# Kernel optimization log

Measured on AMD Instinct MI355X. Metric: run time of the kernel, lower is better.

## Reference

```python
import jax, jax.numpy as jnp
import numpy as np

C, F, CLS, B, HW = 2048, 512, 200, 128, 14
SCALES = (4, 5, 7, 11)
EPS = 1e-5

def _pool_matrix(n, k):
    # PyTorch AdaptiveAvgPool2d bin edges: [floor(i*n/k), ceil((i+1)*n/k))
    P = np.zeros((k, n), np.float32)
    for i in range(k):
        s = (i * n) // k
        e = -((-(i + 1) * n) // k)
        P[i, s:e] = 1.0 / (e - s)
    return jnp.asarray(P)

_PMATS = [_pool_matrix(HW, k) for k in SCALES]

def _bn(x, g, b):
    # BatchNorm with batch statistics (train-mode), biased variance, eps=1e-5
    m = x.mean(0)
    v = x.var(0)
    return (x - m) * jax.lax.rsqrt(v + EPS) * g + b

def _head(h, g1, b1, w1, bi1, g2, b2, w2, bi2):
    # Sequential(BN, Linear, BN, ELU, Linear)
    h = _bn(h, g1, b1) @ w1.T + bi1
    h = jax.nn.elu(_bn(h, g2, b2))
    return h @ w2.T + bi2

def setup_inputs():
    key = jax.random.key(0)
    ks = iter(jax.random.split(key, 16))
    def rn(shape, scale=0.02):
        return jax.random.normal(next(ks), shape, jnp.float32) * scale
    d = {"x": jax.random.normal(next(ks), (B, C, HW, HW), jnp.float32)}
    d.update(g_bn_g=jnp.ones((C,)), g_bn_b=jnp.zeros((C,)), g_w=rn((4, C)), g_b=jnp.zeros((4,)))
    d.update(e_w=rn((C, C)), e_b=jnp.zeros((C,)), e_g=jnp.ones((C,)), e_bb=jnp.zeros((C,)))
    def head(p, din, dh):
        d[p + "_g1"] = jnp.ones((din,)); d[p + "_b1"] = jnp.zeros((din,))
        d[p + "_w1"] = rn((dh, din));   d[p + "_bi1"] = jnp.zeros((dh,))
        d[p + "_g2"] = jnp.ones((dh,)); d[p + "_b2"] = jnp.zeros((dh,))
        d[p + "_w2"] = rn((CLS, dh));   d[p + "_bi2"] = jnp.zeros((CLS,))
    head("hl", C, F)
    head("hh", C, F)
    head("hf", 2 * C, 2 * F)
    return d

def reference(x, g_bn_g, g_bn_b, g_w, g_b, e_w, e_b, e_g, e_bb,
              hl_g1, hl_b1, hl_w1, hl_bi1, hl_g2, hl_b2, hl_w2, hl_bi2,
              hh_g1, hh_b1, hh_w1, hh_bi1, hh_g2, hh_b2, hh_w2, hh_bi2,
              hf_g1, hf_b1, hf_w1, hf_bi1, hf_g2, hf_b2, hf_w2, hf_bi2):
    # Gate: global max pool -> BN -> ELU -> Linear -> hard gumbel-softmax (temp=1,
    # deterministic/eval: straight-through hard argmax over softmax)
    mp = x.max((2, 3))                                              # [B,C]
    logits = jax.nn.elu(_bn(mp, g_bn_g, g_bn_b)) @ g_w.T + g_b      # [B,4]
    soft = jax.nn.softmax(logits, -1)
    hard = jax.nn.one_hot(jnp.argmax(soft, -1), 4, dtype=soft.dtype)
    gw = jax.lax.stop_gradient(hard - soft) + soft                  # [B,4]
    # multi-scale adaptive avg pool (4,5,7,11) then global max per scale — fully batched
    ms = jnp.stack([jnp.einsum('ki,bcij,lj->bckl', P, x, P).max((2, 3)) for P in _PMATS], -1)  # [B,C,4]
    pool = jnp.einsum('bcs,bs->bc', ms, gw)                         # gated weighted sum
    # expert_low: 1x1 conv on 1x1 spatial == linear, then BN2d(batch stats) + ReLU
    xl = jax.nn.relu(_bn(pool @ e_w.T + e_b, e_g, e_bb))
    # NOTE: source computes expert_high(x) then overwrites with self.max(x) -> x_high = global max pool of x
    xh = mp
    xf = jnp.concatenate([xl, xh], -1)
    out_low = _head(xl, hl_g1, hl_b1, hl_w1, hl_bi1, hl_g2, hl_b2, hl_w2, hl_bi2)
    out_high = _head(xh, hh_g1, hh_b1, hh_w1, hh_bi1, hh_g2, hh_b2, hh_w2, hh_bi2)
    out = _head(xf, hf_g1, hf_b1, hf_w1, hf_bi1, hf_g2, hf_b2, hf_w2, hf_bi2)
    return (out_low, out_high, out)
```

## Files before the change

### kernel.cpp

```cpp
#include <hip/hip_runtime.h>
#include <math.h>

#define B_DIM 128
#define C_DIM 2048
#define HW2   196

__global__ __launch_bounds__(256) void pool_max_kernel(
    const float* __restrict__ x, float* __restrict__ mp, float* __restrict__ ms) {
  __shared__ float lds[4][4][208];
  const int tid  = threadIdx.x;
  const int w    = tid >> 6;
  const int lane = tid & 63;
  const int g    = lane >> 4;
  const int c    = lane & 15;
  const size_t waveBase = (size_t)blockIdx.x * 16 + w * 4;

  const float* src = x + waveBase * HW2;
  #pragma unroll
  for (int j = 0; j < 4; ++j) {
    int f = lane + 64 * j;
    if (f < 196) {
      int t = (f * 669) >> 15;
      float4 v = *(const float4*)(src + f * 4);
      *(float4*)&lds[w][t][(f - 49 * t) * 4] = v;
    }
  }

  float xv[14];
  const float* col = &lds[w][g][c];
  #pragma unroll
  for (int r = 0; r < 14; ++r) xv[r] = col[r * 14];

  float cmax = (c < 14) ? xv[0] : -INFINITY;
  #pragma unroll
  for (int r = 1; r < 14; ++r) if (c < 14) cmax = fmaxf(cmax, xv[r]);
  #pragma unroll
  for (int off = 8; off > 0; off >>= 1) cmax = fmaxf(cmax, __shfl_xor(cmax, off));

  float P[15];
  P[0] = 0.f;
  #pragma unroll
  for (int r = 0; r < 14; ++r) P[r + 1] = P[r] + xv[r];

  float sm0, sm1, sm2, sm3;

  {
    constexpr int rs[4] = {0, 3, 7, 10}, re[4] = {4, 7, 11, 14};
    const bool valid = (0x489u >> c) & 1;
    float vmax = -INFINITY;
    #pragma unroll
    for (int i = 0; i < 4; ++i) {
      float v  = P[re[i]] - P[rs[i]];
      float w2 = v + __shfl_down(v, 1);
      float w4 = w2 + __shfl_down(w2, 2);
      vmax = fmaxf(vmax, valid ? w4 : -INFINITY);
    }
    #pragma unroll
    for (int off = 8; off > 0; off >>= 1) vmax = fmaxf(vmax, __shfl_xor(vmax, off));
    sm0 = vmax * 0.0625f;
  }
  {
    constexpr int rs[5] = {0, 2, 5, 8, 11}, re[5] = {3, 6, 9, 12, 14};
    constexpr float srl[5] = {1.f/3.f, 0.25f, 0.25f, 0.25f, 1.f/3.f};
    const bool valid = (0x925u >> c) & 1;
    const bool is3   = (0x801u >> c) & 1;
    const float invc = is3 ? (1.f/3.f) : 0.25f;
    float vmax = -INFINITY;
    #pragma unroll
    for (int i = 0; i < 5; ++i) {
      float v  = P[re[i]] - P[rs[i]];
      float d1 = __shfl_down(v, 1);
      float d2 = __shfl_down(v, 2);
      float w2 = v + d1;
      float w3 = w2 + d2;
      float w4 = w2 + __shfl_down(w2, 2);
      float wv = (is3 ? w3 : w4) * invc * srl[i];
      vmax = fmaxf(vmax, valid ? wv : -INFINITY);
    }
    #pragma unroll
    for (int off = 8; off > 0; off >>= 1) vmax = fmaxf(vmax, __shfl_xor(vmax, off));
    sm1 = vmax;
  }
  {
    constexpr int rs[7] = {0, 2, 4, 6, 8, 10, 12};
    const bool valid = (0x1555u >> c) & 1;
    float vmax = -INFINITY;
    #pragma unroll
    for (int i = 0; i < 7; ++i) {
      float v  = P[rs[i] + 2] - P[rs[i]];
      float w2 = v + __shfl_down(v, 1);
      vmax = fmaxf(vmax, valid ? w2 : -INFINITY);
    }
    #pragma unroll
    for (int off = 8; off > 0; off >>= 1) vmax = fmaxf(vmax, __shfl_xor(vmax, off));
    sm2 = vmax * 0.25f;
  }
  {
    constexpr int rs[11] = {0, 1, 2, 3, 5, 6, 7, 8, 10, 11, 12};
    constexpr int re[11] = {2, 3, 4, 6, 7, 8, 9, 11, 12, 13, 14};
    constexpr float srl[11] = {0.5f, 0.5f, 0.5f, 1.f/3.f, 0.5f, 0.5f, 0.5f,
                               1.f/3.f, 0.5f, 0.5f, 0.5f};
    const bool valid = (0x1DEFu >> c) & 1;
    const bool is3   = (0x108u >> c) & 1;
    const float invc = is3 ? (1.f/3.f) : 0.5f;
    float vmax = -INFINITY;
    #pragma unroll
    for (int i = 0; i < 11; ++i) {
      float v  = P[re[i]] - P[rs[i]];
      float d1 = __shfl_down(v, 1);
      float d2 = __shfl_down(v, 2);
      float w2 = v + d1;
      float w3 = w2 + d2;
      float wv = (is3 ? w3 : w2) * invc * srl[i];
      vmax = fmaxf(vmax, valid ? wv : -INFINITY);
    }
    #pragma unroll
    for (int off = 8; off > 0; off >>= 1) vmax = fmaxf(vmax, __shfl_xor(vmax, off));
    sm3 = vmax;
  }

  if (c == 0) {
    size_t T = waveBase + g;
    mp[T] = cmax;
    *(float4*)&ms[T * 4] = make_float4(sm0, sm1, sm2, sm3);
  }
}

__global__ __launch_bounds__(256) void statsmp_kernel(
    const float* __restrict__ mp,
    const float* __restrict__ hh_g1, const float* __restrict__ hh_b1,
    const float* __restrict__ hf_g1, const float* __restrict__ hf_b1,
    float* __restrict__ mean_mp, float* __restrict__ rstd_mp,
    float* __restrict__ s_h, float* __restrict__ t_h,
    float* __restrict__ sf2, float* __restrict__ tf2) {
  const int ci = threadIdx.x & 15;
  const int g  = threadIdx.x >> 4;
  const int c  = blockIdx.x * 16 + ci;
  float s = 0.f, q = 0.f;
  #pragma unroll
  for (int r = 0; r < 8; ++r) {
    float v = mp[(size_t)(g * 8 + r) * C_DIM + c];
    s += v; q += v * v;
  }
  __shared__ float ss[16][16], qq[16][16];
  ss[g][ci] = s; qq[g][ci] = q;
  __syncthreads();
  if (g == 0) {
    float S = 0.f, Q = 0.f;
    #pragma unroll
    for (int j = 0; j < 16; ++j) { S += ss[j][ci]; Q += qq[j][ci]; }
    float m = S * (1.f / B_DIM);
    float var = Q * (1.f / B_DIM) - m * m;
    if (var < 0.f) var = 0.f;
    float r = rsqrtf(var + 1e-5f);
    mean_mp[c] = m; rstd_mp[c] = r;
    float a = r * hh_g1[c];        s_h[c] = a; t_h[c] = hh_b1[c] - m * a;
    float b = r * hf_g1[2048 + c]; sf2[c] = b; tf2[c] = hf_b1[2048 + c] - m * b;
  }
}

__global__ void gate_select_kernel(
    const float* __restrict__ mp,
    const float* __restrict__ mean, const float* __restrict__ rstd,
    const float* __restrict__ gg, const float* __restrict__ gb,
    const float* __restrict__ gw, const float* __restrict__ gbias,
    const float* __restrict__ ms, float* __restrict__ pool) {
  const int b = blockIdx.x;
  const int t = threadIdx.x;
  float s0 = 0.f, s1 = 0.f, s2 = 0.f, s3 = 0.f;
  for (int c = t; c < C_DIM; c += 256) {
    float v = mp[(size_t)b * C_DIM + c];
    float xn = (v - mean[c]) * rstd[c] * gg[c] + gb[c];
    float e = xn > 0.f ? xn : expm1f(xn);
    s0 += e * gw[c];
    s1 += e * gw[C_DIM + c];
    s2 += e * gw[2 * C_DIM + c];
    s3 += e * gw[3 * C_DIM + c];
  }
  __shared__ float red[4][256];
  __shared__ int ssel;
  red[0][t] = s0; red[1][t] = s1; red[2][t] = s2; red[3][t] = s3;
  __syncthreads();
  for (int st = 128; st > 0; st >>= 1) {
    if (t < st) {
      red[0][t] += red[0][t + st];
      red[1][t] += red[1][t + st];
      red[2][t] += red[2][t + st];
      red[3][t] += red[3][t + st];
    }
    __syncthreads();
  }
  if (t == 0) {
    float best = red[0][0] + gbias[0];
    int bi = 0;
    for (int j = 1; j < 4; ++j) {
      float l = red[j][0] + gbias[j];
      if (l > best) { best = l; bi = j; }
    }
    ssel = bi;
  }
  __syncthreads();
  const int sel = ssel;
  for (int c = t; c < C_DIM; c += 256)
    pool[(size_t)b * C_DIM + c] = ms[((size_t)b * C_DIM + c) * 4 + sel];
}

__global__ __launch_bounds__(256) void gemm_e_kernel(
    const float* __restrict__ A, const float* __restrict__ W,
    float* __restrict__ P) {
  __shared__ float As[32][68];
  __shared__ float Bs[32][68];
  const int t = threadIdx.x;
  const int m0 = blockIdx.y << 6;
  const int n0 = blockIdx.x << 6;
  const int kbeg = blockIdx.z << 8;
  const int lr = t >> 3;
  const int lk4 = (t & 7) << 2;
  const int tx = t & 15, ty = t >> 4;
  float acc[4][4] = {{0.f}};
  for (int k0 = kbeg; k0 < kbeg + 256; k0 += 32) {
    float4 a0 = *(const float4*)&A[(size_t)(m0 + lr) * 2048 + k0 + lk4];
    float4 a1 = *(const float4*)&A[(size_t)(m0 + lr + 32) * 2048 + k0 + lk4];
    float4 b0 = *(const float4*)&W[(size_t)(n0 + lr) * 2048 + k0 + lk4];
    float4 b1 = *(const float4*)&W[(size_t)(n0 + lr + 32) * 2048 + k0 + lk4];
    __syncthreads();
    As[lk4 + 0][lr] = a0.x; As[lk4 + 1][lr] = a0.y; As[lk4 + 2][lr] = a0.z; As[lk4 + 3][lr] = a0.w;
    As[lk4 + 0][lr + 32] = a1.x; As[lk4 + 1][lr + 32] = a1.y; As[lk4 + 2][lr + 32] = a1.z; As[lk4 + 3][lr + 32] = a1.w;
    Bs[lk4 + 0][lr] = b0.x; Bs[lk4 + 1][lr] = b0.y; Bs[lk4 + 2][lr] = b0.z; Bs[lk4 + 3][lr] = b0.w;
    Bs[lk4 + 0][lr + 32] = b1.x; Bs[lk4 + 1][lr + 32] = b1.y; Bs[lk4 + 2][lr + 32] = b1.z; Bs[lk4 + 3][lr + 32] = b1.w;
    __syncthreads();
    #pragma unroll
    for (int kk = 0; kk < 32; ++kk) {
      float4 av = *(const float4*)&As[kk][ty << 2];
      float4 bv = *(const float4*)&Bs[kk][tx << 2];
      acc[0][0] = fmaf(av.x, bv.x, acc[0][0]); acc[0][1] = fmaf(av.x, bv.y, acc[0][1]);
      acc[0][2] = fmaf(av.x, bv.z, acc[0][2]); acc[0][3] = fmaf(av.x, bv.w, acc[0][3]);
      acc[1][0] = fmaf(av.y, bv.x, acc[1][0]); acc[1][1] = fmaf(av.y, bv.y, acc[1][1]);
      acc[1][2] = fmaf(av.y, bv.z, acc[1][2]); acc[1][3] = fmaf(av.y, bv.w, acc[1][3]);
      acc[2][0] = fmaf(av.z, bv.x, acc[2][0]); acc[2][1] = fmaf(av.z, bv.y, acc[2][1]);
      acc[2][2] = fmaf(av.z, bv.z, acc[2][2]); acc[2][3] = fmaf(av.z, bv.w, acc[2][3]);
      acc[3][0] = fmaf(av.w, bv.x, acc[3][0]); acc[3][1] = fmaf(av.w, bv.y, acc[3][1]);
      acc[3][2] = fmaf(av.w, bv.z, acc[3][2]); acc[3][3] = fmaf(av.w, bv.w, acc[3][3]);
    }
  }
  float* Pz = P + ((size_t)blockIdx.z << 18);
  #pragma unroll
  for (int i = 0; i < 4; ++i) {
    int m = m0 + (ty << 2) + i;
    #pragma unroll
    for (int j = 0; j < 4; ++j)
      Pz[(size_t)m * 2048 + n0 + (tx << 2) + j] = acc[i][j];
  }
}

__global__ __launch_bounds__(256) void expert_fused_kernel(
    const float* __restrict__ Pe, const float* __restrict__ e_b,
    const float* __restrict__ e_g, const float* __restrict__ e_bb,
    const float* __restrict__ hl_g1, const float* __restrict__ hl_b1,
    const float* __restrict__ hf_g1, const float* __restrict__ hf_b1,
    float* __restrict__ xl,
    float* __restrict__ s_l, float* __restrict__ t_l,
    float* __restrict__ sf1, float* __restrict__ tf1) {
  const int ci = threadIdx.x & 15;
  const int g  = threadIdx.x >> 4;
  const int c  = blockIdx.x * 16 + ci;
  float v[8];
  float s = 0.f, q = 0.f;
  const float bias = e_b[c];
  #pragma unroll
  for (int r = 0; r < 8; ++r) {
    const size_t row = g * 8 + r;
    float acc = bias;
    #pragma unroll
    for (int z = 0; z < 8; ++z)
      acc += Pe[((size_t)z << 18) + row * 2048 + c];
    v[r] = acc; s += acc; q += acc * acc;
  }
  __shared__ float ss[16][16], qq[16][16];
  __shared__ float sm[16], sr[16];
  ss[g][ci] = s; qq[g][ci] = q;
  __syncthreads();
  if (g == 0) {
    float S = 0.f, Q = 0.f;
    #pragma unroll
    for (int j = 0; j < 16; ++j) { S += ss[j][ci]; Q += qq[j][ci]; }
    float m = S * (1.f / B_DIM);
    float var = Q * (1.f / B_DIM) - m * m;
    if (var < 0.f) var = 0.f;
    sm[ci] = m; sr[ci] = rsqrtf(var + 1e-5f);
  }
  __syncthreads();
  const float m = sm[ci], rst = sr[ci];
  const float eg = e_g[c], eb2 = e_bb[c];
  float s2 = 0.f, q2 = 0.f;
  #pragma unroll
  for (int r = 0; r < 8; ++r) {
    float xv = fmaxf((v[r] - m) * rst * eg + eb2, 0.f);
    xl[(size_t)(g * 8 + r) * 2048 + c] = xv;
    s2 += xv; q2 += xv * xv;
  }
  __syncthreads();
  ss[g][ci] = s2; qq[g][ci] = q2;
  __syncthreads();
  if (g == 0) {
    float S = 0.f, Q = 0.f;
    #pragma unroll
    for (int j = 0; j < 16; ++j) { S += ss[j][ci]; Q += qq[j][ci]; }
    float mm = S * (1.f / B_DIM);
    float var = Q * (1.f / B_DIM) - mm * mm;
    if (var < 0.f) var = 0.f;
    float rr = rsqrtf(var + 1e-5f);
    float a = rr * hl_g1[c]; s_l[c] = a; t_l[c] = hl_b1[c] - mm * a;
    float b = rr * hf_g1[c]; sf1[c] = b; tf1[c] = hf_b1[c] - mm * b;
  }
}

__global__ __launch_bounds__(256) void gemm_w1_kernel(
    const float* __restrict__ xl, const float* __restrict__ mp,
    const float* __restrict__ s_l, const float* __restrict__ t_l,
    const float* __restrict__ s_h, const float* __restrict__ t_h,
    const float* __restrict__ sf1, const float* __restrict__ tf1,
    const float* __restrict__ sf2, const float* __restrict__ tf2,
    const float* __restrict__ hl_w1, const float* __restrict__ hh_w1,
    const float* __restrict__ hf_w1,
    float* __restrict__ P_l, float* __restrict__ P_h, float* __restrict__ P_f) {
  const int jx = blockIdx.x;
  const int z  = blockIdx.z;
  const float *A, *S, *T, *Wt;
  float* P;
  int N, K, n0, kA, kW, Kc;
  if (jx < 8) {
    N = 512; K = 2048; Kc = 128; Wt = hl_w1; n0 = jx << 6;
    kW = z * 128; kA = kW; A = xl; S = s_l; T = t_l;
    P = P_l + ((size_t)z << 16);
  } else if (jx < 16) {
    N = 512; K = 2048; Kc = 128; Wt = hh_w1; n0 = (jx - 8) << 6;
    kW = z * 128; kA = kW; A = mp; S = s_h; T = t_h;
    P = P_h + ((size_t)z << 16);
  } else {
    N = 1024; K = 4096; Kc = 256; Wt = hf_w1; n0 = (jx - 16) << 6;
    kW = z * 256;
    if (kW >= 2048) { A = mp; S = sf2; T = tf2; kA = kW - 2048; }
    else            { A = xl; S = sf1; T = tf1; kA = kW; }
    P = P_f + ((size_t)z << 17);
  }
  const int m0 = blockIdx.y << 6;
  __shared__ float As[32][68];
  __shared__ float Bs[32][68];
  const int t = threadIdx.x;
  const int lr = t >> 3;
  const int lk4 = (t & 7) << 2;
  const int tx = t & 15, ty = t >> 4;
  float acc[4][4] = {{0.f}};
  for (int k0 = 0; k0 < Kc; k0 += 32) {
    const int ka = kA + k0 + lk4;
    float4 a0 = *(const float4*)&A[(size_t)(m0 + lr) * 2048 + ka];
    float4 a1 = *(const float4*)&A[(size_t)(m0 + lr + 32) * 2048 + ka];
    float4 s4 = *(const float4*)&S[ka];
    float4 t4 = *(const float4*)&T[ka];
    a0.x = fmaf(a0.x, s4.x, t4.x); a0.y = fmaf(a0.y, s4.y, t4.y);
    a0.z = fmaf(a0.z, s4.z, t4.z); a0.w = fmaf(a0.w, s4.w, t4.w);
    a1.x = fmaf(a1.x, s4.x, t4.x); a1.y = fmaf(a1.y, s4.y, t4.y);
    a1.z = fmaf(a1.z, s4.z, t4.z); a1.w = fmaf(a1.w, s4.w, t4.w);
    const int kw = kW + k0 + lk4;
    float4 b0 = *(const float4*)&Wt[(size_t)(n0 + lr) * K + kw];
    float4 b1 = *(const float4*)&Wt[(size_t)(n0 + lr + 32) * K + kw];
    __syncthreads();
    As[lk4 + 0][lr] = a0.x; As[lk4 + 1][lr] = a0.y; As[lk4 + 2][lr] = a0.z; As[lk4 + 3][lr] = a0.w;
    As[lk4 + 0][lr + 32] = a1.x; As[lk4 + 1][lr + 32] = a1.y; As[lk4 + 2][lr + 32] = a1.z; As[lk4 + 3][lr + 32] = a1.w;
    Bs[lk4 + 0][lr] = b0.x; Bs[lk4 + 1][lr] = b0.y; Bs[lk4 + 2][lr] = b0.z; Bs[lk4 + 3][lr] = b0.w;
    Bs[lk4 + 0][lr + 32] = b1.x; Bs[lk4 + 1][lr + 32] = b1.y; Bs[lk4 + 2][lr + 32] = b1.z; Bs[lk4 + 3][lr + 32] = b1.w;
    __syncthreads();
    #pragma unroll
    for (int kk = 0; kk < 32; ++kk) {
      float4 av = *(const float4*)&As[kk][ty << 2];
      float4 bv = *(const float4*)&Bs[kk][tx << 2];
      acc[0][0] = fmaf(av.x, bv.x, acc[0][0]); acc[0][1] = fmaf(av.x, bv.y, acc[0][1]);
      acc[0][2] = fmaf(av.x, bv.z, acc[0][2]); acc[0][3] = fmaf(av.x, bv.w, acc[0][3]);
      acc[1][0] = fmaf(av.y, bv.x, acc[1][0]); acc[1][1] = fmaf(av.y, bv.y, acc[1][1]);
      acc[1][2] = fmaf(av.y, bv.z, acc[1][2]); acc[1][3] = fmaf(av.y, bv.w, acc[1][3]);
      acc[2][0] = fmaf(av.z, bv.x, acc[2][0]); acc[2][1] = fmaf(av.z, bv.y, acc[2][1]);
      acc[2][2] = fmaf(av.z, bv.z, acc[2][2]); acc[2][3] = fmaf(av.z, bv.w, acc[2][3]);
      acc[3][0] = fmaf(av.w, bv.x, acc[3][0]); acc[3][1] = fmaf(av.w, bv.y, acc[3][1]);
      acc[3][2] = fmaf(av.w, bv.z, acc[3][2]); acc[3][3] = fmaf(av.w, bv.w, acc[3][3]);
    }
  }
  #pragma unroll
  for (int i = 0; i < 4; ++i) {
    int m = m0 + (ty << 2) + i;
    #pragma unroll
    for (int j = 0; j < 4; ++j)
      P[(size_t)m * N + n0 + (tx << 2) + j] = acc[i][j];
  }
}

__global__ __launch_bounds__(256) void heads_fused_kernel(
    const float* __restrict__ P_l, const float* __restrict__ P_h,
    const float* __restrict__ P_f,
    const float* __restrict__ bl1, const float* __restrict__ bh1,
    const float* __restrict__ bf1,
    const float* __restrict__ g2l, const float* __restrict__ b2l,
    const float* __restrict__ g2h, const float* __restrict__ b2h,
    const float* __restrict__ g2f, const float* __restrict__ b2f,
    float* __restrict__ a2_l, float* __restrict__ a2_h, float* __restrict__ a2_f) {
  const int ci = threadIdx.x & 15;
  const int g  = threadIdx.x >> 4;
  const int cj = blockIdx.x * 16 + ci;
  const float *P, *bi, *g2, *b2;
  float* out;
  int N, cc;
  if (cj < 512)       { P = P_l; bi = bl1; g2 = g2l; b2 = b2l; out = a2_l; N = 512;  cc = cj; }
  else if (cj < 1024) { P = P_h; bi = bh1; g2 = g2h; b2 = b2h; out = a2_h; N = 512;  cc = cj - 512; }
  else                { P = P_f; bi = bf1; g2 = g2f; b2 = b2f; out = a2_f; N = 1024; cc = cj - 1024; }
  const size_t sstride = (size_t)N * 128;
  float v[8];
  float s = 0.f, q = 0.f;
  const float bias = bi[cc];
  #pragma unroll
  for (int r = 0; r < 8; ++r) {
    const size_t row = g * 8 + r;
    float acc = bias;
    #pragma unroll
    for (int z = 0; z < 16; ++z)
      acc += P[(size_t)z * sstride + row * N + cc];
    v[r] = acc; s += acc; q += acc * acc;
  }
  __shared__ float ss[16][16], qq[16][16];
  __shared__ float sm[16], sr[16];
  ss[g][ci] = s; qq[g][ci] = q;
  __syncthreads();
  if (g == 0) {
    float S = 0.f, Q = 0.f;
    #pragma unroll
    for (int j = 0; j < 16; ++j) { S += ss[j][ci]; Q += qq[j][ci]; }
    float m = S * (1.f / B_DIM);
    float var = Q * (1.f / B_DIM) - m * m;
    if (var < 0.f) var = 0.f;
    sm[ci] = m; sr[ci] = rsqrtf(var + 1e-5f);
  }
  __syncthreads();
  const float m = sm[ci], rr = sr[ci];
  const float gg = g2[cc], bb = b2[cc];
  #pragma unroll
  for (int r = 0; r < 8; ++r) {
    float xn = (v[r] - m) * rr * gg + bb;
    out[(size_t)(g * 8 + r) * N + cc] = xn > 0.f ? xn : expm1f(xn);
  }
}

__global__ __launch_bounds__(256) void gemm_w2_kernel(
    const float* __restrict__ a2_l, const float* __restrict__ a2_h,
    const float* __restrict__ a2_f,
    const float* __restrict__ hl_w2, const float* __restrict__ hh_w2,
    const float* __restrict__ hf_w2,
    float* __restrict__ Pw) {
  const int jx = blockIdx.x;
  const int z  = blockIdx.z;
  const float *A, *Wt;
  int K, Kc, pOff, n0;
  if (jx < 4)      { A = a2_l; Wt = hl_w2; K = 512;  Kc = 64;  pOff = 0;     n0 = jx << 6; }
  else if (jx < 8) { A = a2_h; Wt = hh_w2; K = 512;  Kc = 64;  pOff = 25600; n0 = (jx - 4) << 6; }
  else             { A = a2_f; Wt = hf_w2; K = 1024; Kc = 128; pOff = 51200; n0 = (jx - 8) << 6; }
  const int kbeg = z * Kc;
  const int m0 = blockIdx.y << 6;
  __shared__ float As[32][68];
  __shared__ float Bs[32][68];
  const int t = threadIdx.x;
  const int lr = t >> 3;
  const int lk4 = (t & 7) << 2;
  const int tx = t & 15, ty = t >> 4;
  float acc[4][4] = {{0.f}};
  const float4 z4 = make_float4(0.f, 0.f, 0.f, 0.f);
  for (int k0 = kbeg; k0 < kbeg + Kc; k0 += 32) {
    float4 a0 = *(const float4*)&A[(size_t)(m0 + lr) * K + k0 + lk4];
    float4 a1 = *(const float4*)&A[(size_t)(m0 + lr + 32) * K + k0 + lk4];
    int n1 = n0 + lr, n2 = n0 + lr + 32;
    float4 b0 = (n1 < 200) ? *(const float4*)&Wt[(size_t)n1 * K + k0 + lk4] : z4;
    float4 b1 = (n2 < 200) ? *(const float4*)&Wt[(size_t)n2 * K + k0 + lk4] : z4;
    __syncthreads();
    As[lk4 + 0][lr] = a0.x; As[lk4 + 1][lr] = a0.y; As[lk4 + 2][lr] = a0.z; As[lk4 + 3][lr] = a0.w;
    As[lk4 + 0][lr + 32] = a1.x; As[lk4 + 1][lr + 32] = a1.y; As[lk4 + 2][lr + 32] = a1.z; As[lk4 + 3][lr + 32] = a1.w;
    Bs[lk4 + 0][lr] = b0.x; Bs[lk4 + 1][lr] = b0.y; Bs[lk4 + 2][lr] = b0.z; Bs[lk4 + 3][lr] = b0.w;
    Bs[lk4 + 0][lr + 32] = b1.x; Bs[lk4 + 1][lr + 32] = b1.y; Bs[lk4 + 2][lr + 32] = b1.z; Bs[lk4 + 3][lr + 32] = b1.w;
    __syncthreads();
    #pragma unroll
    for (int kk = 0; kk < 32; ++kk) {
      float4 av = *(const float4*)&As[kk][ty << 2];
      float4 bv = *(const float4*)&Bs[kk][tx << 2];
      acc[0][0] = fmaf(av.x, bv.x, acc[0][0]); acc[0][1] = fmaf(av.x, bv.y, acc[0][1]);
      acc[0][2] = fmaf(av.x, bv.z, acc[0][2]); acc[0][3] = fmaf(av.x, bv.w, acc[0][3]);
      acc[1][0] = fmaf(av.y, bv.x, acc[1][0]); acc[1][1] = fmaf(av.y, bv.y, acc[1][1]);
      acc[1][2] = fmaf(av.y, bv.z, acc[1][2]); acc[1][3] = fmaf(av.y, bv.w, acc[1][3]);
      acc[2][0] = fmaf(av.z, bv.x, acc[2][0]); acc[2][1] = fmaf(av.z, bv.y, acc[2][1]);
      acc[2][2] = fmaf(av.z, bv.z, acc[2][2]); acc[2][3] = fmaf(av.z, bv.w, acc[2][3]);
      acc[3][0] = fmaf(av.w, bv.x, acc[3][0]); acc[3][1] = fmaf(av.w, bv.y, acc[3][1]);
      acc[3][2] = fmaf(av.w, bv.z, acc[3][2]); acc[3][3] = fmaf(av.w, bv.w, acc[3][3]);
    }
  }
  float* Pz = Pw + (size_t)z * 76800 + pOff;
  #pragma unroll
  for (int i = 0; i < 4; ++i) {
    int m = m0 + (ty << 2) + i;
    #pragma unroll
    for (int j = 0; j < 4; ++j) {
      int n = n0 + (tx << 2) + j;
      if (n < 200) Pz[(size_t)m * 200 + n] = acc[i][j];
    }
  }
}

__global__ void reduce_out_kernel(const float* __restrict__ P,
                                  const float* __restrict__ bl,
                                  const float* __restrict__ bh,
                                  const float* __restrict__ bf,
                                  float* __restrict__ out) {
  int i = blockIdx.x * 256 + threadIdx.x;
  if (i >= 76800) return;
  int job = i / 25600;
  int n = (i - job * 25600) % 200;
  float s = (job == 0) ? bl[n] : (job == 1) ? bh[n] : bf[n];
  for (int z = 0; z < 8; ++z) s += P[(size_t)z * 76800 + i];
  out[i] = s;
}

extern "C" void kernel_launch(void* const* d_in, const int* in_sizes, int n_in,
                              void* d_out, int out_size, void* d_ws, size_t ws_size,
                              hipStream_t stream) {
  const float* x      = (const float*)d_in[0];
  const float* g_bn_g = (const float*)d_in[1];
  const float* g_bn_b = (const float*)d_in[2];
  const float* g_w    = (const float*)d_in[3];
  const float* g_b    = (const float*)d_in[4];
  const float* e_w    = (const float*)d_in[5];
  const float* e_b    = (const float*)d_in[6];
  const float* e_g    = (const float*)d_in[7];
  const float* e_bb   = (const float*)d_in[8];
  const float* hl_g1  = (const float*)d_in[9];
  const float* hl_b1  = (const float*)d_in[10];
  const float* hl_w1  = (const float*)d_in[11];
  const float* hl_bi1 = (const float*)d_in[12];
  const float* hl_g2  = (const float*)d_in[13];
  const float* hl_b2  = (const float*)d_in[14];
  const float* hl_w2  = (const float*)d_in[15];
  const float* hl_bi2 = (const float*)d_in[16];
  const float* hh_g1  = (const float*)d_in[17];
  const float* hh_b1  = (const float*)d_in[18];
  const float* hh_w1  = (const float*)d_in[19];
  const float* hh_bi1 = (const float*)d_in[20];
  const float* hh_g2  = (const float*)d_in[21];
  const float* hh_b2  = (const float*)d_in[22];
  const float* hh_w2  = (const float*)d_in[23];
  const float* hh_bi2 = (const float*)d_in[24];
  const float* hf_g1  = (const float*)d_in[25];
  const float* hf_b1  = (const float*)d_in[26];
  const float* hf_w1  = (const float*)d_in[27];
  const float* hf_bi1 = (const float*)d_in[28];
  const float* hf_g2  = (const float*)d_in[29];
  const float* hf_b2  = (const float*)d_in[30];
  const float* hf_w2  = (const float*)d_in[31];
  const float* hf_bi2 = (const float*)d_in[32];
  float* out = (float*)d_out;

  float* W = (float*)d_ws;
  const size_t BC = (size_t)B_DIM * C_DIM;
  float* mp   = W;
  float* ms   = mp + BC;
  float* pool = ms + BC * 4;
  float* xl   = pool + BC;
  float* a2_l = xl + BC;
  float* a2_h = a2_l + 128 * 512;
  float* a2_f = a2_h + 128 * 512;
  float* st   = a2_f + 128 * 1024;
  float* mean_mp = st;           float* rstd_mp = st + 2048;
  float* s_h  = st + 2 * 2048;   float* t_h  = st + 3 * 2048;
  float* sf2  = st + 4 * 2048;   float* tf2  = st + 5 * 2048;
  float* s_l  = st + 6 * 2048;   float* t_l  = st + 7 * 2048;
  float* sf1  = st + 8 * 2048;   float* tf1  = st + 9 * 2048;
  float* P_e  = st + 10 * 2048;
  float* P_l2 = P_e + 8 * BC;
  float* P_hh = P_l2 + (size_t)16 * 65536;
  float* P_f  = P_hh + (size_t)16 * 65536;
  float* P_w2 = P_e;

  pool_max_kernel<<<16384, 256, 0, stream>>>(x, mp, ms);

  statsmp_kernel<<<128, 256, 0, stream>>>(mp, hh_g1, hh_b1, hf_g1, hf_b1,
                                          mean_mp, rstd_mp, s_h, t_h, sf2, tf2);

  gate_select_kernel<<<128, 256, 0, stream>>>(mp, mean_mp, rstd_mp, g_bn_g, g_bn_b,
                                              g_w, g_b, ms, pool);

  gemm_e_kernel<<<dim3(32, 2, 8), 256, 0, stream>>>(pool, e_w, P_e);

  expert_fused_kernel<<<128, 256, 0, stream>>>(P_e, e_b, e_g, e_bb,
                                               hl_g1, hl_b1, hf_g1, hf_b1,
                                               xl, s_l, t_l, sf1, tf1);

  gemm_w1_kernel<<<dim3(32, 2, 16), 256, 0, stream>>>(
      xl, mp, s_l, t_l, s_h, t_h, sf1, tf1, sf2, tf2,
      hl_w1, hh_w1, hf_w1, P_l2, P_hh, P_f);

  heads_fused_kernel<<<128, 256, 0, stream>>>(
      P_l2, P_hh, P_f, hl_bi1, hh_bi1, hf_bi1,
      hl_g2, hl_b2, hh_g2, hh_b2, hf_g2, hf_b2,
      a2_l, a2_h, a2_f);

  gemm_w2_kernel<<<dim3(12, 2, 8), 256, 0, stream>>>(
      a2_l, a2_h, a2_f, hl_w2, hh_w2, hf_w2, P_w2);

  reduce_out_kernel<<<300, 256, 0, stream>>>(P_w2, hl_bi2, hh_bi2, hf_bi2, out);
}
```

Baseline: 158.6 us.

## Port expert and head-W1 GEMMs to bf16 MFMA with swizzled LDS tiles

Replaces the fp32 FMA tiled GEMMs for the expert linear and the three head first-layer linears with bf16 MFMA 16x16x32 kernels. Each block now covers all 128 batch rows with XOR-swizzled LDS tiles, converting fp32 inputs to bf16 on load. The grid drops the M dimension but keeps split-K. This aims to cut the ALU cost of the small GEMMs, at the price of bf16 rounding of activations and weights, which risks accuracy against the fp32 reference.

```diff
diff --git a/kernel.cpp b/kernel.cpp
--- a/kernel.cpp
+++ b/kernel.cpp
@@ -4,6 +4,15 @@
 #define B_DIM 128
 #define C_DIM 2048
 #define HW2   196
+
+typedef __attribute__((ext_vector_type(8))) short bf16x8;
+typedef __attribute__((ext_vector_type(4))) float f32x4;
+
+__device__ __forceinline__ unsigned short f2bf(float f) {
+  unsigned u = __float_as_uint(f);
+  u += 0x7FFFu + ((u >> 16) & 1u);
+  return (unsigned short)(u >> 16);
+}
 
 __global__ __launch_bounds__(256) void pool_max_kernel(
     const float* __restrict__ x, float* __restrict__ mp, float* __restrict__ ms) {
@@ -205,51 +214,103 @@
     pool[(size_t)b * C_DIM + c] = ms[((size_t)b * C_DIM + c) * 4 + sel];
 }
 
-__global__ __launch_bounds__(256) void gemm_e_kernel(
+__global__ __launch_bounds__(256) void gemm_e_mfma_kernel(
     const float* __restrict__ A, const float* __restrict__ W,
     float* __restrict__ P) {
-  __shared__ float As[32][68];
-  __shared__ float Bs[32][68];
+  __shared__ __align__(16) short As[128 * 64];
+  __shared__ __align__(16) short Bs[64 * 64];
   const int t = threadIdx.x;
-  const int m0 = blockIdx.y << 6;
   const int n0 = blockIdx.x << 6;
-  const int kbeg = blockIdx.z << 8;
-  const int lr = t >> 3;
-  const int lk4 = (t & 7) << 2;
-  const int tx = t & 15, ty = t >> 4;
-  float acc[4][4] = {{0.f}};
-  for (int k0 = kbeg; k0 < kbeg + 256; k0 += 32) {
-    float4 a0 = *(const float4*)&A[(size_t)(m0 + lr) * 2048 + k0 + lk4];
-    float4 a1 = *(const float4*)&A[(size_t)(m0 + lr + 32) * 2048 + k0 + lk4];
-    float4 b0 = *(const float4*)&W[(size_t)(n0 + lr) * 2048 + k0 + lk4];
-    float4 b1 = *(const float4*)&W[(size_t)(n0 + lr + 32) * 2048 + k0 + lk4];
+  const int kbeg = blockIdx.y << 8;
+
+  const int rowA = t >> 1, koffA = (t & 1) << 5;
+  const int rowB = t >> 2, koffB = (t & 3) << 4;
+
+  const int lane = t & 63, wav = t >> 6;
+  const int r = lane & 15, kb = lane >> 4;
+  int aoff[2][2], boff[2][4];
+  #pragma unroll
+  for (int kk = 0; kk < 2; ++kk) {
+    #pragma unroll
+    for (int mi = 0; mi < 2; ++mi) {
+      int row = wav * 32 + mi * 16 + r;
+      aoff[kk][mi] = row * 128 + ((((kk << 2) + kb) ^ (row & 7)) << 4);
+    }
+    #pragma unroll
+    for (int ni = 0; ni < 4; ++ni) {
+      int cl = ni * 16 + r;
+      boff[kk][ni] = cl * 128 + ((((kk << 2) + kb) ^ (cl & 7)) << 4);
+    }
+  }
+
+  f32x4 acc[2][4];
+  #pragma unroll
+  for (int mi = 0; mi < 2; ++mi)
+    #pragma unroll
+    for (int ni = 0; ni < 4; ++ni)
+      acc[mi][ni] = (f32x4){0.f, 0.f, 0.f, 0.f};
+
+  for (int kt = 0; kt < 256; kt += 64) {
+    const int kg = kbeg + kt;
+    const float4* ap = (const float4*)&A[(size_t)rowA * 2048 + kg + koffA];
+    const float4* bp = (const float4*)&W[(size_t)(n0 + rowB) * 2048 + kg + koffB];
+    float4 fa[8], fb[4];
+    #pragma unroll
+    for (int j = 0; j < 8; ++j) fa[j] = ap[j];
+    #pragma unroll
+    for (int j = 0; j < 4; ++j) fb[j] = bp[j];
     __syncthreads();
-    As[lk4 + 0][lr] = a0.x; As[lk4 + 1][lr] = a0.y; As[lk4 + 2][lr] = a0.z; As[lk4 + 3][lr] = a0.w;
-    As[lk4 + 0][lr + 32] = a1.x; As[lk4 + 1][lr + 32] = a1.y; As[lk4 + 2][lr + 32] = a1.z; As[lk4 + 3][lr + 32] = a1.w;
-    Bs[lk4 + 0][lr] = b0.x; Bs[lk4 + 1][lr] = b0.y; Bs[lk4 + 2][lr] = b0.z; Bs[lk4 + 3][lr] = b0.w;
-    Bs[lk4 + 0][lr + 32] = b1.x; Bs[lk4 + 1][lr + 32] = b1.y; Bs[lk4 + 2][lr + 32] = b1.z; Bs[lk4 + 3][lr + 32] = b1.w;
+    #pragma unroll
+    for (int j = 0; j < 4; ++j) {
+      bf16x8 v;
+      v[0] = (short)f2bf(fa[2*j].x);   v[1] = (short)f2bf(fa[2*j].y);
+      v[2] = (short)f2bf(fa[2*j].z);   v[3] = (short)f2bf(fa[2*j].w);
+      v[4] = (short)f2bf(fa[2*j+1].x); v[5] = (short)f2bf(fa[2*j+1].y);
+      v[6] = (short)f2bf(fa[2*j+1].z); v[7] = (short)f2bf(fa[2*j+1].w);
+      int slot = (koffA >> 3) + j;
+      *(bf16x8*)((char*)As + rowA * 128 + ((slot ^ (rowA & 7)) << 4)) = v;
+    }
+    #pragma unroll
+    for (int j = 0; j < 2; ++j) {
+      bf16x8 v;
+      v[0] = (short)f2bf(fb[2*j].x);   v[1] = (short)f2bf(fb[2*j].y);
+      v[2] = (short)f2bf(fb[2*j].z);   v[3] = (short)f2bf(fb[2*j].w);
+      v[4] = (short)f2bf(fb[2*j+1].x); v[5] = (short)f2bf(fb[2*j+1].y);
+      v[6] = (short)f2bf(fb[2*j+1].z); v[7] = (short)f2bf(fb[2*j+1].w);
+      int slot = (koffB >> 3) + j;
+      *(bf16x8*)((char*)Bs + rowB * 128 + ((slot ^ (rowB & 7)) << 4)) = v;
+    }
     __syncthreads();
     #pragma unroll
-    for (int kk = 0; kk < 32; ++kk) {
-      float4 av = *(const float4*)&As[kk][ty << 2];
-      float4 bv = *(const float4*)&Bs[kk][tx << 2];
-      acc[0][0] = fmaf(av.x, bv.x, acc[0][0]); acc[0][1] = fmaf(av.x, bv.y, acc[0][1]);
-      acc[0][2] = fmaf(av.x, bv.z, acc[0][2]); acc[0][3] = fmaf(av.x, bv.w, acc[0][3]);
-      acc[1][0] = fmaf(av.y, bv.x, acc[1][0]); acc[1][1] = fmaf(av.y, bv.y, acc[1][1]);
-      acc[1][2] = fmaf(av.y, bv.z, acc[1][2]); acc[1][3] = fmaf(av.y, bv.w, acc[1][3]);
-      acc[2][0] = fmaf(av.z, bv.x, acc[2][0]); acc[2][1] = fmaf(av.z, bv.y, acc[2][1]);
-      acc[2][2] = fmaf(av.z, bv.z, acc[2][2]); acc[2][3] = fmaf(av.z, bv.w, acc[2][3]);
-      acc[3][0] = fmaf(av.w, bv.x, acc[3][0]); acc[3][1] = fmaf(av.w, bv.y, acc[3][1]);
-      acc[3][2] = fmaf(av.w, bv.z, acc[3][2]); acc[3][3] = fmaf(av.w, bv.w, acc[3][3]);
-    }
-  }
-  float* Pz = P + ((size_t)blockIdx.z << 18);
-  #pragma unroll
-  for (int i = 0; i < 4; ++i) {
-    int m = m0 + (ty << 2) + i;
-    #pragma unroll
-    for (int j = 0; j < 4; ++j)
-      Pz[(size_t)m * 2048 + n0 + (tx << 2) + j] = acc[i][j];
+    for (int kk = 0; kk < 2; ++kk) {
+      bf16x8 a0 = *(bf16x8*)((char*)As + aoff[kk][0]);
+      bf16x8 a1 = *(bf16x8*)((char*)As + aoff[kk][1]);
+      bf16x8 b0 = *(bf16x8*)((char*)Bs + boff[kk][0]);
+      bf16x8 b1 = *(bf16x8*)((char*)Bs + boff[kk][1]);
+      bf16x8 b2 = *(bf16x8*)((char*)Bs + boff[kk][2]);
+      bf16x8 b3 = *(bf16x8*)((char*)Bs + boff[kk][3]);
+      acc[0][0] = __builtin_amdgcn_mfma_f32_16x16x32_bf16(a0, b0, acc[0][0], 0, 0, 0);
+      acc[0][1] = __builtin_amdgcn_mfma_f32_16x16x32_bf16(a0, b1, acc[0][1], 0, 0, 0);
+      acc[0][2] = __builtin_amdgcn_mfma_f32_16x16x32_bf16(a0, b2, acc[0][2], 0, 0, 0);
+      acc[0][3] = __builtin_amdgcn_mfma_f32_16x16x32_bf16(a0, b3, acc[0][3], 0, 0, 0);
+      acc[1][0] = __builtin_amdgcn_mfma_f32_16x16x32_bf16(a1, b0, acc[1][0], 0, 0, 0);
+      acc[1][1] = __builtin_amdgcn_mfma_f32_16x16x32_bf16(a1, b1, acc[1][1], 0, 0, 0);
+      acc[1][2] = __builtin_amdgcn_mfma_f32_16x16x32_bf16(a1, b2, acc[1][2], 0, 0, 0);
+      acc[1][3] = __builtin_amdgcn_mfma_f32_16x16x32_bf16(a1, b3, acc[1][3], 0, 0, 0);
+    }
+  }
+
+  float* Pz = P + ((size_t)blockIdx.y << 18);
+  #pragma unroll
+  for (int mi = 0; mi < 2; ++mi) {
+    int row = wav * 32 + mi * 16 + kb * 4;
+    #pragma unroll
+    for (int ni = 0; ni < 4; ++ni) {
+      int cl = n0 + ni * 16 + r;
+      #pragma unroll
+      for (int g2 = 0; g2 < 4; ++g2)
+        Pz[(size_t)(row + g2) * 2048 + cl] = acc[mi][ni][g2];
+    }
   }
 }
 
@@ -315,7 +376,7 @@
   }
 }
 
-__global__ __launch_bounds__(256) void gemm_w1_kernel(
+__global__ __launch_bounds__(256) void gemm_w1_mfma_kernel(
     const float* __restrict__ xl, const float* __restrict__ mp,
     const float* __restrict__ s_l, const float* __restrict__ t_l,
     const float* __restrict__ s_h, const float* __restrict__ t_h,
@@ -324,73 +385,126 @@
     const float* __restrict__ hl_w1, const float* __restrict__ hh_w1,
     const float* __restrict__ hf_w1,
     float* __restrict__ P_l, float* __restrict__ P_h, float* __restrict__ P_f) {
+  __shared__ __align__(16) short As[128 * 64];
+  __shared__ __align__(16) short Bs[64 * 64];
   const int jx = blockIdx.x;
-  const int z  = blockIdx.z;
+  const int z  = blockIdx.y;
   const float *A, *S, *T, *Wt;
   float* P;
-  int N, K, n0, kA, kW, Kc;
+  int N, Kdim, n0, kA0, kW0, Kc;
   if (jx < 8) {
-    N = 512; K = 2048; Kc = 128; Wt = hl_w1; n0 = jx << 6;
-    kW = z * 128; kA = kW; A = xl; S = s_l; T = t_l;
+    N = 512; Kdim = 2048; Kc = 128; Wt = hl_w1; n0 = jx << 6;
+    kW0 = z * 128; kA0 = kW0; A = xl; S = s_l; T = t_l;
     P = P_l + ((size_t)z << 16);
   } else if (jx < 16) {
-    N = 512; K = 2048; Kc = 128; Wt = hh_w1; n0 = (jx - 8) << 6;
-    kW = z * 128; kA = kW; A = mp; S = s_h; T = t_h;
+    N = 512; Kdim = 2048; Kc = 128; Wt = hh_w1; n0 = (jx - 8) << 6;
+    kW0 = z * 128; kA0 = kW0; A = mp; S = s_h; T = t_h;
     P = P_h + ((size_t)z << 16);
   } else {
-    N = 1024; K = 4096; Kc = 256; Wt = hf_w1; n0 = (jx - 16) << 6;
-    kW = z * 256;
-    if (kW >= 2048) { A = mp; S = sf2; T = tf2; kA = kW - 2048; }
-    else            { A = xl; S = sf1; T = tf1; kA = kW; }
+    N = 1024; Kdim = 4096; Kc = 256; Wt = hf_w1; n0 = (jx - 16) << 6;
+    kW0 = z * 256;
+    if (kW0 >= 2048) { A = mp; S = sf2; T = tf2; kA0 = kW0 - 2048; }
+    else             { A = xl; S = sf1; T = tf1; kA0 = kW0; }
     P = P_f + ((size_t)z << 17);
   }
-  const int m0 = blockIdx.y << 6;
-  __shared__ float As[32][68];
-  __shared__ float Bs[32][68];
   const int t = threadIdx.x;
-  const int lr = t >> 3;
-  const int lk4 = (t & 7) << 2;
-  const int tx = t & 15, ty = t >> 4;
-  float acc[4][4] = {{0.f}};
-  for (int k0 = 0; k0 < Kc; k0 += 32) {
-    const int ka = kA + k0 + lk4;
-    float4 a0 = *(const float4*)&A[(size_t)(m0 + lr) * 2048 + ka];
-    float4 a1 = *(const float4*)&A[(size_t)(m0 + lr + 32) * 2048 + ka];
-    float4 s4 = *(const float4*)&S[ka];
-    float4 t4 = *(const float4*)&T[ka];
-    a0.x = fmaf(a0.x, s4.x, t4.x); a0.y = fmaf(a0.y, s4.y, t4.y);
-    a0.z = fmaf(a0.z, s4.z, t4.z); a0.w = fmaf(a0.w, s4.w, t4.w);
-    a1.x = fmaf(a1.x, s4.x, t4.x); a1.y = fmaf(a1.y, s4.y, t4.y);
-    a1.z = fmaf(a1.z, s4.z, t4.z); a1.w = fmaf(a1.w, s4.w, t4.w);
-    const int kw = kW + k0 + lk4;
-    float4 b0 = *(const float4*)&Wt[(size_t)(n0 + lr) * K + kw];
-    float4 b1 = *(const float4*)&Wt[(size_t)(n0 + lr + 32) * K + kw];
+  const int rowA = t >> 1, koffA = (t & 1) << 5;
+  const int rowB = t >> 2, koffB = (t & 3) << 4;
+
+  const int lane = t & 63, wav = t >> 6;
+  const int r = lane & 15, kb = lane >> 4;
+  int aoff[2][2], boff[2][4];
+  #pragma unroll
+  for (int kk = 0; kk < 2; ++kk) {
+    #pragma unroll
+    for (int mi = 0; mi < 2; ++mi) {
+      int row = wav * 32 + mi * 16 + r;
+      aoff[kk][mi] = row * 128 + ((((kk << 2) + kb) ^ (row & 7)) << 4);
+    }
+    #pragma unroll
+    for (int ni = 0; ni < 4; ++ni) {
+      int cl = ni * 16 + r;
+      boff[kk][ni] = cl * 128 + ((((kk << 2) + kb) ^ (cl & 7)) << 4);
+    }
+  }
+
+  f32x4 acc[2][4];
+  #pragma unroll
+  for (int mi = 0; mi < 2; ++mi)
+    #pragma unroll
+    for (int ni = 0; ni < 4; ++ni)
+      acc[mi][ni] = (f32x4){0.f, 0.f, 0.f, 0.f};
+
+  for (int kt = 0; kt < Kc; kt += 64) {
+    const int ka = kA0 + kt + koffA;
+    const float4* ap = (const float4*)&A[(size_t)rowA * 2048 + ka];
+    const float4* sp = (const float4*)&S[ka];
+    const float4* tp = (const float4*)&T[ka];
+    const float4* bp = (const float4*)&Wt[(size_t)(n0 + rowB) * Kdim + kW0 + kt + koffB];
+    float4 fa[8], fb[4];
+    #pragma unroll
+    for (int j = 0; j < 8; ++j) fa[j] = ap[j];
+    #pragma unroll
+    for (int j = 0; j < 8; ++j) {
+      float4 s4 = sp[j], t4 = tp[j];
+      fa[j].x = fmaf(fa[j].x, s4.x, t4.x);
+      fa[j].y = fmaf(fa[j].y, s4.y, t4.y);
+      fa[j].z = fmaf(fa[j].z, s4.z, t4.z);
+      fa[j].w = fmaf(fa[j].w, s4.w, t4.w);
+    }
+    #pragma unroll
+    for (int j = 0; j < 4; ++j) fb[j] = bp[j];
     __syncthreads();
-    As[lk4 + 0][lr] = a0.x; As[lk4 + 1][lr] = a0.y; As[lk4 + 2][lr] = a0.z; As[lk4 + 3][lr] = a0.w;
-    As[lk4 + 0][lr + 32] = a1.x; As[lk4 + 1][lr + 32] = a1.y; As[lk4 + 2][lr + 32] = a1.z; As[lk4 + 3][lr + 32] = a1.w;
-    Bs[lk4 + 0][lr] = b0.x; Bs[lk4 + 1][lr] = b0.y; Bs[lk4 + 2][lr] = b0.z; Bs[lk4 + 3][lr] = b0.w;
-    Bs[lk4 + 0][lr + 32] = b1.x; Bs[lk4 + 1][lr + 32] = b1.y; Bs[lk4 + 2][lr + 32] = b1.z; Bs[lk4 + 3][lr + 32] = b1.w;
+    #pragma unroll
+    for (int j = 0; j < 4; ++j) {
+      bf16x8 v;
+      v[0] = (short)f2bf(fa[2*j].x);   v[1] = (short)f2bf(fa[2*j].y);
+      v[2] = (short)f2bf(fa[2*j].z);   v[3] = (short)f2bf(fa[2*j].w);
+      v[4] = (short)f2bf(fa[2*j+1].x); v[5] = (short)f2bf(fa[2*j+1].y);
+      v[6] = (short)f2bf(fa[2*j+1].z); v[7] = (short)f2bf(fa[2*j+1].w);
+      int slot = (koffA >> 3) + j;
+      *(bf16x8*)((char*)As + rowA * 128 + ((slot ^ (rowA & 7)) << 4)) = v;
+    }
+    #pragma unroll
+    for (int j = 0; j < 2; ++j) {
+      bf16x8 v;
+      v[0] = (short)f2bf(fb[2*j].x);   v[1] = (short)f2bf(fb[2*j].y);
+      v[2] = (short)f2bf(fb[2*j].z);   v[3] = (short)f2bf(fb[2*j].w);
+      v[4] = (short)f2bf(fb[2*j+1].x); v[5] = (short)f2bf(fb[2*j+1].y);
+      v[6] = (short)f2bf(fb[2*j+1].z); v[7] = (short)f2bf(fb[2*j+1].w);
+      int slot = (koffB >> 3) + j;
+      *(bf16x8*)((char*)Bs + rowB * 128 + ((slot ^ (rowB & 7)) << 4)) = v;
+    }
     __syncthreads();
     #pragma unroll
-    for (int kk = 0; kk < 32; ++kk) {
-      float4 av = *(const float4*)&As[kk][ty << 2];
-      float4 bv = *(const float4*)&Bs[kk][tx << 2];
-      acc[0][0] = fmaf(av.x, bv.x, acc[0][0]); acc[0][1] = fmaf(av.x, bv.y, acc[0][1]);
-      acc[0][2] = fmaf(av.x, bv.z, acc[0][2]); acc[0][3] = fmaf(av.x, bv.w, acc[0][3]);
-      acc[1][0] = fmaf(av.y, bv.x, acc[1][0]); acc[1][1] = fmaf(av.y, bv.y, acc[1][1]);
-      acc[1][2] = fmaf(av.y, bv.z, acc[1][2]); acc[1][3] = fmaf(av.y, bv.w, acc[1][3]);
-      acc[2][0] = fmaf(av.z, bv.x, acc[2][0]); acc[2][1] = fmaf(av.z, bv.y, acc[2][1]);
-      acc[2][2] = fmaf(av.z, bv.z, acc[2][2]); acc[2][3] = fmaf(av.z, bv.w, acc[2][3]);
-      acc[3][0] = fmaf(av.w, bv.x, acc[3][0]); acc[3][1] = fmaf(av.w, bv.y, acc[3][1]);
-      acc[3][2] = fmaf(av.w, bv.z, acc[3][2]); acc[3][3] = fmaf(av.w, bv.w, acc[3][3]);
-    }
-  }
-  #pragma unroll
-  for (int i = 0; i < 4; ++i) {
-    int m = m0 + (ty << 2) + i;
-    #pragma unroll
-    for (int j = 0; j < 4; ++j)
-      P[(size_t)m * N + n0 + (tx << 2) + j] = acc[i][j];
+    for (int kk = 0; kk < 2; ++kk) {
+      bf16x8 a0 = *(bf16x8*)((char*)As + aoff[kk][0]);
+      bf16x8 a1 = *(bf16x8*)((char*)As + aoff[kk][1]);
+      bf16x8 b0 = *(bf16x8*)((char*)Bs + boff[kk][0]);
+      bf16x8 b1 = *(bf16x8*)((char*)Bs + boff[kk][1]);
+      bf16x8 b2 = *(bf16x8*)((char*)Bs + boff[kk][2]);
+      bf16x8 b3 = *(bf16x8*)((char*)Bs + boff[kk][3]);
+      acc[0][0] = __builtin_amdgcn_mfma_f32_16x16x32_bf16(a0, b0, acc[0][0], 0, 0, 0);
+      acc[0][1] = __builtin_amdgcn_mfma_f32_16x16x32_bf16(a0, b1, acc[0][1], 0, 0, 0);
+      acc[0][2] = __builtin_amdgcn_mfma_f32_16x16x32_bf16(a0, b2, acc[0][2], 0, 0, 0);
+      acc[0][3] = __builtin_amdgcn_mfma_f32_16x16x32_bf16(a0, b3, acc[0][3], 0, 0, 0);
+      acc[1][0] = __builtin_amdgcn_mfma_f32_16x16x32_bf16(a1, b0, acc[1][0], 0, 0, 0);
+      acc[1][1] = __builtin_amdgcn_mfma_f32_16x16x32_bf16(a1, b1, acc[1][1], 0, 0, 0);
+      acc[1][2] = __builtin_amdgcn_mfma_f32_16x16x32_bf16(a1, b2, acc[1][2], 0, 0, 0);
+      acc[1][3] = __builtin_amdgcn_mfma_f32_16x16x32_bf16(a1, b3, acc[1][3], 0, 0, 0);
+    }
+  }
+
+  #pragma unroll
+  for (int mi = 0; mi < 2; ++mi) {
+    int row = wav * 32 + mi * 16 + kb * 4;
+    #pragma unroll
+    for (int ni = 0; ni < 4; ++ni) {
+      int cl = n0 + ni * 16 + r;
+      #pragma unroll
+      for (int g2 = 0; g2 < 4; ++g2)
+        P[(size_t)(row + g2) * N + cl] = acc[mi][ni][g2];
+    }
   }
 }
 
@@ -590,13 +704,13 @@
   gate_select_kernel<<<128, 256, 0, stream>>>(mp, mean_mp, rstd_mp, g_bn_g, g_bn_b,
                                               g_w, g_b, ms, pool);
 
-  gemm_e_kernel<<<dim3(32, 2, 8), 256, 0, stream>>>(pool, e_w, P_e);
+  gemm_e_mfma_kernel<<<dim3(32, 8), 256, 0, stream>>>(pool, e_w, P_e);
 
   expert_fused_kernel<<<128, 256, 0, stream>>>(P_e, e_b, e_g, e_bb,
                                                hl_g1, hl_b1, hf_g1, hf_b1,
                                                xl, s_l, t_l, sf1, tf1);
 
-  gemm_w1_kernel<<<dim3(32, 2, 16), 256, 0, stream>>>(
+  gemm_w1_mfma_kernel<<<dim3(32, 16), 256, 0, stream>>>(
       xl, mp, s_l, t_l, s_h, t_h, sf1, tf1, sf2, tf2,
       hl_w1, hh_w1, hf_w1, P_l2, P_hh, P_f);
 
```

New measurement: 139.5 us. 1.14x faster.
